# Optimization experiments

Measured on AMD Instinct MI355X. Metric: run time of the kernel, lower is better.

## Reference

```python
import jax, jax.numpy as jnp
import numpy as np

MAX_DIFF = 0.5


def setup_inputs() -> dict:
    key = jax.random.key(0)
    actions = jax.random.normal(key, (4096, 256, 64), dtype=jnp.float32)
    return {"actions": actions}


def reference(actions):
    # actions: [B, T, A]
    # diffs along time, clamped, then reconstruct via prefix sum from actions[:, 0]
    diffs = jnp.clip(jnp.diff(actions, axis=1), -MAX_DIFF, MAX_DIFF)  # [B, T-1, A]
    rest = actions[:, :1, :] + jnp.cumsum(diffs, axis=1)              # [B, T-1, A]
    return jnp.concatenate([actions[:, :1, :], rest], axis=1)         # [B, T, A]
```

## Files before the change

### kernel.cpp

```cpp
#include <hip/hip_runtime.h>
#include <hip/hip_bf16.h>


typedef float v4f __attribute__((ext_vector_type(4)));

__device__ __forceinline__ float clip05(float d) {
    return fminf(fmaxf(d, -0.5f), 0.5f);
}

__global__ __launch_bounds__(256, 8) void smooth_scan(
    const float* __restrict__ in, float* __restrict__ out) {
    constexpr int T    = 256;
    constexpr int R4   = 16;
    constexpr int SEG  = 8;
    constexpr int NSEG = 32;
    constexpr int AH   = 8;

    __shared__ v4f lds_x0[AH];
    __shared__ v4f lds_last[NSEG][AH];
    __shared__ v4f lds_tot[NSEG][AH];

    const int bh  = blockIdx.x;
    const int b   = bh >> 1;
    const int hf  = bh & 1;
    const int a4  = threadIdx.x & (AH - 1);
    const int seg = threadIdx.x >> 3;

    const size_t base = ((size_t)b * T + (size_t)seg * SEG) * R4 + (size_t)hf * AH + a4;
    const v4f* __restrict__ ip = (const v4f*)in + base;
    v4f*       __restrict__ op = (v4f*)out + base;

    v4f v[SEG];
#pragma unroll
    for (int i = 0; i < SEG; ++i) v[i] = __builtin_nontemporal_load(ip + i * R4);

    lds_last[seg][a4] = v[SEG - 1];
    if (seg == 0) lds_x0[a4] = v[0];
    __syncthreads();

    v4f prev = (seg != 0) ? lds_last[seg - 1][a4] : v[0];

    v4f run = (v4f){0.f, 0.f, 0.f, 0.f};
#pragma unroll
    for (int i = 0; i < SEG; ++i) {
        const v4f cur = v[i];
        run.x += clip05(cur.x - prev.x);
        run.y += clip05(cur.y - prev.y);
        run.z += clip05(cur.z - prev.z);
        run.w += clip05(cur.w - prev.w);
        prev = cur;
        v[i] = run;
    }

    lds_tot[seg][a4] = run;
    __syncthreads();

    v4f off = lds_x0[a4];
    for (int s = 0; s < seg; ++s) off += lds_tot[s][a4];

#pragma unroll
    for (int i = 0; i < SEG; ++i)
        __builtin_nontemporal_store(off + v[i], op + i * R4);
}

extern "C" void kernel_launch(void* const* d_in, const int* in_sizes, int n_in,
                              void* d_out, int out_size, void* d_ws, size_t ws_size,
                              hipStream_t stream) {
    const float* in = (const float*)d_in[0];
    float* out = (float*)d_out;

    constexpr int B = 4096;
    smooth_scan<<<B * 2, 256, 0, stream>>>(in, out);
}
```

Measured before the change: 419.9 us.

## Stage whole batch in LDS for fully coalesced loads and stores

Each block now handles a full batch row set (256x64 floats). It loads the data into a 64KB LDS tile with contiguous coalesced vector loads, performs the segmented clip-diff scan in LDS, and writes back coalesced with per-segment offsets. This replaces the strided per-thread half-row accesses and halves the grid. The large LDS footprint limits how many blocks fit per CU and adds extra barriers, which may reduce latency hiding.

```diff
diff --git a/kernel.cpp b/kernel.cpp
--- a/kernel.cpp
+++ b/kernel.cpp
@@ -8,59 +8,63 @@
     return fminf(fmaxf(d, -0.5f), 0.5f);
 }
 
-__global__ __launch_bounds__(256, 8) void smooth_scan(
+__device__ __forceinline__ v4f clipdiff(v4f a, v4f b) {
+    v4f r;
+    r.x = clip05(a.x - b.x);
+    r.y = clip05(a.y - b.y);
+    r.z = clip05(a.z - b.z);
+    r.w = clip05(a.w - b.w);
+    return r;
+}
+
+__global__ __launch_bounds__(256) void smooth_scan(
     const float* __restrict__ in, float* __restrict__ out) {
-    constexpr int T    = 256;
-    constexpr int R4   = 16;
-    constexpr int SEG  = 8;
-    constexpr int NSEG = 32;
-    constexpr int AH   = 8;
+    constexpr int T  = 256;
+    constexpr int A4 = 16;
+    constexpr int NV = T * A4;
 
-    __shared__ v4f lds_x0[AH];
-    __shared__ v4f lds_last[NSEG][AH];
-    __shared__ v4f lds_tot[NSEG][AH];
+    __shared__ v4f tile[NV];
+    __shared__ v4f tot[16][A4];
+    __shared__ v4f offt[16][A4];
 
-    const int bh  = blockIdx.x;
-    const int b   = bh >> 1;
-    const int hf  = bh & 1;
-    const int a4  = threadIdx.x & (AH - 1);
-    const int seg = threadIdx.x >> 3;
-
-    const size_t base = ((size_t)b * T + (size_t)seg * SEG) * R4 + (size_t)hf * AH + a4;
+    const int tid = threadIdx.x;
+    const size_t base = (size_t)blockIdx.x * NV;
     const v4f* __restrict__ ip = (const v4f*)in + base;
     v4f*       __restrict__ op = (v4f*)out + base;
 
-    v4f v[SEG];
 #pragma unroll
-    for (int i = 0; i < SEG; ++i) v[i] = __builtin_nontemporal_load(ip + i * R4);
-
-    lds_last[seg][a4] = v[SEG - 1];
-    if (seg == 0) lds_x0[a4] = v[0];
+    for (int k = 0; k < 16; ++k)
+        tile[tid + 256 * k] = __builtin_nontemporal_load(ip + tid + 256 * k);
     __syncthreads();
 
-    v4f prev = (seg != 0) ? lds_last[seg - 1][a4] : v[0];
+    const int a4  = tid & 15;
+    const int seg = tid >> 4;
+    const v4f first = tile[a4];
+    v4f prev = (seg == 0) ? first : tile[(seg * 16 - 1) * A4 + a4];
+    __syncthreads();
 
     v4f run = (v4f){0.f, 0.f, 0.f, 0.f};
 #pragma unroll
-    for (int i = 0; i < SEG; ++i) {
-        const v4f cur = v[i];
-        run.x += clip05(cur.x - prev.x);
-        run.y += clip05(cur.y - prev.y);
-        run.z += clip05(cur.z - prev.z);
-        run.w += clip05(cur.w - prev.w);
+    for (int i = 0; i < 16; ++i) {
+        const int idx = (seg * 16 + i) * A4 + a4;
+        const v4f cur = tile[idx];
+        run += clipdiff(cur, prev);
         prev = cur;
-        v[i] = run;
+        tile[idx] = run;
     }
-
-    lds_tot[seg][a4] = run;
+    tot[seg][a4] = run;
     __syncthreads();
 
-    v4f off = lds_x0[a4];
-    for (int s = 0; s < seg; ++s) off += lds_tot[s][a4];
+    v4f off = first;
+    for (int s = 0; s < seg; ++s) off += tot[s][a4];
+    offt[seg][a4] = off;
+    __syncthreads();
 
 #pragma unroll
-    for (int i = 0; i < SEG; ++i)
-        __builtin_nontemporal_store(off + v[i], op + i * R4);
+    for (int k = 0; k < 16; ++k) {
+        const int f = tid + 256 * k;
+        __builtin_nontemporal_store(tile[f] + offt[k][tid & 15], op + f);
+    }
 }
 
 extern "C" void kernel_launch(void* const* d_in, const int* in_sizes, int n_in,
@@ -70,5 +74,5 @@
     float* out = (float*)d_out;
 
     constexpr int B = 4096;
-    smooth_scan<<<B * 2, 256, 0, stream>>>(in, out);
+    smooth_scan<<<B, 256, 0, stream>>>(in, out);
 }
```

Result: no change. 419.2 us (-0.2%).
